# Kernel tuning notes

Measured on AMD Instinct MI355X. Metric: run time of the kernel, lower is better.

The kernel has to match this reference:

```python
import jax, jax.numpy as jnp
import numpy as np

POOL = 7  # pool_size (7x7)


def setup_inputs() -> dict:
    key = jax.random.key(0)
    kb, kw, k2, k3, k4, k5 = jax.random.split(key, 6)
    B, N, C = 2, 1000, 256
    # boxes: (y1, x1, y2, x2) normalized, guaranteed y1<y2, x1<x2, inside [0,1]
    yx = jax.random.uniform(kb, (B, N, 2), dtype=jnp.float32)
    wh = jax.random.uniform(kw, (B, N, 2), dtype=jnp.float32) * 0.3 + 0.01
    y1x1 = yx * (1.0 - wh)
    y2x2 = y1x1 + wh
    boxes = jnp.concatenate([y1x1, y2x2], axis=-1)
    image_shape = jnp.array([1024, 1024, 3], dtype=jnp.int32)
    feat2 = jax.random.normal(k2, (B, 256, 256, C), dtype=jnp.float32)
    feat3 = jax.random.normal(k3, (B, 128, 128, C), dtype=jnp.float32)
    feat4 = jax.random.normal(k4, (B, 64, 64, C), dtype=jnp.float32)
    feat5 = jax.random.normal(k5, (B, 32, 32, C), dtype=jnp.float32)
    return dict(boxes=boxes, image_shape=image_shape,
                feat2=feat2, feat3=feat3, feat4=feat4, feat5=feat5)


def _crop_and_resize(feat, boxes, box_idx, P):
    """TF tf.image.crop_and_resize semantics (bilinear, extrapolation_value=0).

    feat: [B, H, W, C]; boxes: [M, 4] normalized; box_idx: [M] int32.
    Returns [M, P, P, C].
    """
    H, W = feat.shape[1], feat.shape[2]
    y1, x1, y2, x2 = (boxes[:, 0], boxes[:, 1], boxes[:, 2], boxes[:, 3])
    i = jnp.arange(P, dtype=feat.dtype)
    # sample coordinates in source-pixel space (P > 1 branch of TF kernel)
    ys = y1[:, None] * (H - 1) + i[None, :] * ((y2 - y1) * (H - 1) / (P - 1))[:, None]  # [M,P]
    xs = x1[:, None] * (W - 1) + i[None, :] * ((x2 - x1) * (W - 1) / (P - 1))[:, None]  # [M,P]

    def corners(s, L):
        s0 = jnp.floor(s)
        frac = s - s0
        i0 = jnp.clip(s0.astype(jnp.int32), 0, L - 1)
        i1 = jnp.clip(i0 + 1, 0, L - 1)
        valid = (s >= 0) & (s <= L - 1)
        return i0, i1, frac, valid

    y0, y1i, fy, vy = corners(ys, H)
    x0, x1i, fx, vx = corners(xs, W)
    b = box_idx[:, None, None]
    # 4 bilinear corners, each gathered as [M, P, P, C]
    v00 = feat[b, y0[:, :, None], x0[:, None, :]]
    v01 = feat[b, y0[:, :, None], x1i[:, None, :]]
    v10 = feat[b, y1i[:, :, None], x0[:, None, :]]
    v11 = feat[b, y1i[:, :, None], x1i[:, None, :]]
    fy_ = fy[:, :, None, None]
    fx_ = fx[:, None, :, None]
    top = v00 * (1 - fx_) + v01 * fx_
    bot = v10 * (1 - fx_) + v11 * fx_
    out = top * (1 - fy_) + bot * fy_
    mask = (vy[:, :, None] & vx[:, None, :])[..., None]
    return jnp.where(mask, out, jnp.zeros((), feat.dtype))


def reference(boxes, image_shape, feat2, feat3, feat4, feat5):
    B, N = boxes.shape[0], boxes.shape[1]
    P = POOL
    boxes_flat = boxes.reshape(B * N, 4)
    box_idx = jnp.repeat(jnp.arange(B, dtype=jnp.int32), N)
    h = boxes_flat[:, 2] - boxes_flat[:, 0]
    w = boxes_flat[:, 3] - boxes_flat[:, 1]
    area = (image_shape[0] * image_shape[1]).astype(jnp.float32)
    # FPN level routing: level = clip(4 + round(log2(sqrt(wh)*sqrt(area)/224)), 2, 5)
    lvl = jnp.log(jnp.sqrt(w * h) * jnp.sqrt(area) / 224.0) / jnp.log(2.0)
    lvl = jnp.clip(4.0 + jnp.round(lvl), 2.0, 5.0).astype(jnp.int32)
    feats = (feat2, feat3, feat4, feat5)
    C = feat2.shape[-1]
    out = jnp.zeros((B * N, P, P, C), dtype=feat2.dtype)
    for i, level in enumerate((2, 3, 4, 5)):
        crop = _crop_and_resize(feats[i], boxes_flat, box_idx, P)
        sel = (lvl == level)[:, None, None, None]
        out = jnp.where(sel, crop, out)
    # original sorts by 100000*batch + box_id to restore order; our dense
    # select already produces the original (batch, box) ordering.
    return out.reshape(B, N, P, P, C)
```

## Files before the change

### kernel.cpp

```cpp
#include <hip/hip_runtime.h>

#define POOL 7

__global__ __launch_bounds__(256) void roialign_kernel(
    const float* __restrict__ boxes,
    const int*   __restrict__ image_shape,
    const float* __restrict__ feat2,
    const float* __restrict__ feat3,
    const float* __restrict__ feat4,
    const float* __restrict__ feat5,
    float*       __restrict__ out,
    int B, int N, int C, int total_points)
{
    const int P = POOL;
    const int wave = threadIdx.x >> 6;
    const int lane = threadIdx.x & 63;
    const int pt   = blockIdx.x * 4 + wave;
    if (pt >= total_points) return;

    const int m  = pt / (P * P);
    const int pp = pt - m * (P * P);
    const int py = pp / P;
    const int px = pp - py * P;
    const int b  = m / N;

    const float y1 = boxes[m * 4 + 0];
    const float x1 = boxes[m * 4 + 1];
    const float y2 = boxes[m * 4 + 2];
    const float x2 = boxes[m * 4 + 3];
    const float h  = y2 - y1;
    const float w  = x2 - x1;
    const float area = (float)(image_shape[0] * image_shape[1]);

    const float lvlf = logf(sqrtf(w * h) * sqrtf(area) / 224.0f) * 1.4426950408889634f;
    const int lvl = (int)fminf(fmaxf(4.0f + rintf(lvlf), 2.0f), 5.0f);

    const float* feat;
    int H;
    switch (lvl) {
        case 2:  feat = feat2; H = 256; break;
        case 3:  feat = feat3; H = 128; break;
        case 4:  feat = feat4; H = 64;  break;
        default: feat = feat5; H = 32;  break;
    }
    const int W = H;

    const float sy = y1 * (float)(H - 1) + (float)py * (h * (float)(H - 1) / (float)(P - 1));
    const float sx = x1 * (float)(W - 1) + (float)px * (w * (float)(W - 1) / (float)(P - 1));

    const float y0f = floorf(sy);
    const float fy  = sy - y0f;
    int yi0 = (int)y0f;
    yi0 = yi0 < 0 ? 0 : (yi0 > H - 1 ? H - 1 : yi0);
    int yi1 = yi0 + 1 > H - 1 ? H - 1 : yi0 + 1;
    const bool vy = (sy >= 0.0f) && (sy <= (float)(H - 1));

    const float x0f = floorf(sx);
    const float fx  = sx - x0f;
    int xi0 = (int)x0f;
    xi0 = xi0 < 0 ? 0 : (xi0 > W - 1 ? W - 1 : xi0);
    int xi1 = xi0 + 1 > W - 1 ? W - 1 : xi0 + 1;
    const bool vx = (sx >= 0.0f) && (sx <= (float)(W - 1));

    const bool valid = vy && vx;

    const int c = lane * 4;
    if (c >= C) return;

    const size_t planeB = (size_t)H * W * C;
    const float* fb = feat + (size_t)b * planeB;

    const size_t i00 = ((size_t)yi0 * W + xi0) * C + c;
    const size_t i01 = ((size_t)yi0 * W + xi1) * C + c;
    const size_t i10 = ((size_t)yi1 * W + xi0) * C + c;
    const size_t i11 = ((size_t)yi1 * W + xi1) * C + c;

    float4 r;
    if (valid) {
        const float4 v00 = *(const float4*)(fb + i00);
        const float4 v01 = *(const float4*)(fb + i01);
        const float4 v10 = *(const float4*)(fb + i10);
        const float4 v11 = *(const float4*)(fb + i11);

        const float gx = 1.0f - fx, gy = 1.0f - fy;
        r.x = (v00.x * gx + v01.x * fx) * gy + (v10.x * gx + v11.x * fx) * fy;
        r.y = (v00.y * gx + v01.y * fx) * gy + (v10.y * gx + v11.y * fx) * fy;
        r.z = (v00.z * gx + v01.z * fx) * gy + (v10.z * gx + v11.z * fx) * fy;
        r.w = (v00.w * gx + v01.w * fx) * gy + (v10.w * gx + v11.w * fx) * fy;
    } else {
        r.x = r.y = r.z = r.w = 0.0f;
    }

    *(float4*)(out + (size_t)pt * C + c) = r;
}

extern "C" void kernel_launch(void* const* d_in, const int* in_sizes, int n_in,
                              void* d_out, int out_size, void* d_ws, size_t ws_size,
                              hipStream_t stream) {
    const float* boxes       = (const float*)d_in[0];
    const int*   image_shape = (const int*)  d_in[1];
    const float* feat2       = (const float*)d_in[2];
    const float* feat3       = (const float*)d_in[3];
    const float* feat4       = (const float*)d_in[4];
    const float* feat5       = (const float*)d_in[5];
    float*       out         = (float*)d_out;

    const int B = 2;
    const int C = 256;
    const int N = in_sizes[0] / (B * 4);
    const int total_points = B * N * POOL * POOL;

    const int points_per_block = 4;
    const int grid = (total_points + points_per_block - 1) / points_per_block;

    roialign_kernel<<<grid, 256, 0, stream>>>(
        boxes, image_shape, feat2, feat3, feat4, feat5, out,
        B, N, C, total_points);
}
```

Before: 254.6 us.

## Process a full output row per wave with nontemporal stores

Each wave now computes all seven x-samples of one output row instead of a single point, so the box decode, level routing and y-interpolation setup run once per row rather than once per point. The four corner loads are issued unconditionally, and validity is applied by multiplying with a 0/1 mask instead of branching. Output writes use nontemporal stores so the large write stream does not pollute the cache. The grid shrinks sevenfold, which reduces the number of waves available to hide latency, and the unconditional loads can fetch data that is then masked away.

```diff
diff --git a/kernel.cpp b/kernel.cpp
--- a/kernel.cpp
+++ b/kernel.cpp
@@ -1,8 +1,11 @@
 #include <hip/hip_runtime.h>
 
 #define POOL 7
+#define CCH  256
 
-__global__ __launch_bounds__(256) void roialign_kernel(
+typedef float f32x4 __attribute__((ext_vector_type(4)));
+
+__global__ __launch_bounds__(256) void roialign_rows(
     const float* __restrict__ boxes,
     const int*   __restrict__ image_shape,
     const float* __restrict__ feat2,
@@ -10,18 +13,16 @@
     const float* __restrict__ feat4,
     const float* __restrict__ feat5,
     float*       __restrict__ out,
-    int B, int N, int C, int total_points)
+    int N, int total_rows)
 {
     const int P = POOL;
     const int wave = threadIdx.x >> 6;
     const int lane = threadIdx.x & 63;
-    const int pt   = blockIdx.x * 4 + wave;
-    if (pt >= total_points) return;
+    const int task = blockIdx.x * 4 + wave;
+    if (task >= total_rows) return;
 
-    const int m  = pt / (P * P);
-    const int pp = pt - m * (P * P);
-    const int py = pp / P;
-    const int px = pp - py * P;
+    const int m  = task / P;
+    const int py = task - m * P;
     const int b  = m / N;
 
     const float y1 = boxes[m * 4 + 0];
@@ -46,52 +47,46 @@
     const int W = H;
 
     const float sy = y1 * (float)(H - 1) + (float)py * (h * (float)(H - 1) / (float)(P - 1));
-    const float sx = x1 * (float)(W - 1) + (float)px * (w * (float)(W - 1) / (float)(P - 1));
-
     const float y0f = floorf(sy);
     const float fy  = sy - y0f;
     int yi0 = (int)y0f;
     yi0 = yi0 < 0 ? 0 : (yi0 > H - 1 ? H - 1 : yi0);
-    int yi1 = yi0 + 1 > H - 1 ? H - 1 : yi0 + 1;
+    const int yi1 = yi0 + 1 > H - 1 ? H - 1 : yi0 + 1;
     const bool vy = (sy >= 0.0f) && (sy <= (float)(H - 1));
 
-    const float x0f = floorf(sx);
-    const float fx  = sx - x0f;
-    int xi0 = (int)x0f;
-    xi0 = xi0 < 0 ? 0 : (xi0 > W - 1 ? W - 1 : xi0);
-    int xi1 = xi0 + 1 > W - 1 ? W - 1 : xi0 + 1;
-    const bool vx = (sx >= 0.0f) && (sx <= (float)(W - 1));
+    const int c = lane * 4;
 
-    const bool valid = vy && vx;
+    const float* __restrict__ fb   = feat + (size_t)b * ((size_t)H * W * CCH);
+    const float* __restrict__ row0 = fb + (size_t)yi0 * W * CCH + c;
+    const float* __restrict__ row1 = fb + (size_t)yi1 * W * CCH + c;
+    float* __restrict__ orow = out + ((size_t)m * (P * P) + (size_t)py * P) * CCH + c;
 
-    const int c = lane * 4;
-    if (c >= C) return;
+    const float xbase = x1 * (float)(W - 1);
+    const float xstep = w * (float)(W - 1) / (float)(P - 1);
+    const float gy = 1.0f - fy;
 
-    const size_t planeB = (size_t)H * W * C;
-    const float* fb = feat + (size_t)b * planeB;
+#pragma unroll
+    for (int px = 0; px < P; ++px) {
+        const float sx  = xbase + (float)px * xstep;
+        const float x0f = floorf(sx);
+        const float fx  = sx - x0f;
+        int xi0 = (int)x0f;
+        xi0 = xi0 < 0 ? 0 : (xi0 > W - 1 ? W - 1 : xi0);
+        const int xi1 = xi0 + 1 > W - 1 ? W - 1 : xi0 + 1;
+        const bool valid = vy && (sx >= 0.0f) && (sx <= (float)(W - 1));
 
-    const size_t i00 = ((size_t)yi0 * W + xi0) * C + c;
-    const size_t i01 = ((size_t)yi0 * W + xi1) * C + c;
-    const size_t i10 = ((size_t)yi1 * W + xi0) * C + c;
-    const size_t i11 = ((size_t)yi1 * W + xi1) * C + c;
+        const f32x4 v00 = *(const f32x4*)(row0 + xi0 * CCH);
+        const f32x4 v01 = *(const f32x4*)(row0 + xi1 * CCH);
+        const f32x4 v10 = *(const f32x4*)(row1 + xi0 * CCH);
+        const f32x4 v11 = *(const f32x4*)(row1 + xi1 * CCH);
 
-    float4 r;
-    if (valid) {
-        const float4 v00 = *(const float4*)(fb + i00);
-        const float4 v01 = *(const float4*)(fb + i01);
-        const float4 v10 = *(const float4*)(fb + i10);
-        const float4 v11 = *(const float4*)(fb + i11);
+        const float gx = 1.0f - fx;
+        f32x4 r = (v00 * gx + v01 * fx) * gy + (v10 * gx + v11 * fx) * fy;
+        const float vm = valid ? 1.0f : 0.0f;
+        r *= vm;
 
-        const float gx = 1.0f - fx, gy = 1.0f - fy;
-        r.x = (v00.x * gx + v01.x * fx) * gy + (v10.x * gx + v11.x * fx) * fy;
-        r.y = (v00.y * gx + v01.y * fx) * gy + (v10.y * gx + v11.y * fx) * fy;
-        r.z = (v00.z * gx + v01.z * fx) * gy + (v10.z * gx + v11.z * fx) * fy;
-        r.w = (v00.w * gx + v01.w * fx) * gy + (v10.w * gx + v11.w * fx) * fy;
-    } else {
-        r.x = r.y = r.z = r.w = 0.0f;
+        __builtin_nontemporal_store(r, (f32x4*)(orow + px * CCH));
     }
-
-    *(float4*)(out + (size_t)pt * C + c) = r;
 }
 
 extern "C" void kernel_launch(void* const* d_in, const int* in_sizes, int n_in,
@@ -106,14 +101,13 @@
     float*       out         = (float*)d_out;
 
     const int B = 2;
-    const int C = 256;
     const int N = in_sizes[0] / (B * 4);
-    const int total_points = B * N * POOL * POOL;
+    const int total_rows = B * N * POOL;
 
-    const int points_per_block = 4;
-    const int grid = (total_points + points_per_block - 1) / points_per_block;
+    const int rows_per_block = 4;
+    const int grid = (total_rows + rows_per_block - 1) / rows_per_block;
 
-    roialign_kernel<<<grid, 256, 0, stream>>>(
+    roialign_rows<<<grid, 256, 0, stream>>>(
         boxes, image_shape, feat2, feat3, feat4, feat5, out,
-        B, N, C, total_points);
+        N, total_rows);
 }
```

Result: no change. 255.6 us (+0.4%).
